# Performance work log

Measured on AMD Instinct MI355X. Metric: run time of the kernel, lower is better.

Reference implementation:

```python
import jax, jax.numpy as jnp
import numpy as np

N, E, IN_DIM, OUT_DIM, SEM_DIM = 50000, 800000, 128, 128, 128
EPS = 1e-8


def setup_inputs() -> dict:
    key = jax.random.key(0)
    k = jax.random.split(key, 8)
    x = jax.random.normal(k[0], (N, IN_DIM), dtype=jnp.float32)
    edge_index = jax.random.randint(k[1], (2, E), 0, N, dtype=jnp.int64)
    semantic_vec = jax.random.normal(k[2], (N, SEM_DIM), dtype=jnp.float32)
    s = 1.0 / np.sqrt(IN_DIM)
    W_src = jax.random.uniform(k[3], (OUT_DIM, IN_DIM), jnp.float32, -s, s)
    b_src = jax.random.uniform(k[4], (OUT_DIM,), jnp.float32, -s, s)
    W_dst = jax.random.uniform(k[5], (OUT_DIM, IN_DIM), jnp.float32, -s, s)
    b_dst = jax.random.uniform(k[6], (OUT_DIM,), jnp.float32, -s, s)
    return {"x": x, "edge_index": edge_index, "semantic_vec": semantic_vec,
            "W_src": W_src, "b_src": b_src, "W_dst": W_dst, "b_dst": b_dst}


def _scatter_softmax(sim, dst, num_segments):
    # numerically stable segment-wise softmax over edges grouped by dst
    seg_max = jax.ops.segment_max(sim, dst, num_segments=num_segments)
    seg_max = jnp.where(jnp.isneginf(seg_max), 0.0, seg_max)
    e = jnp.exp(sim - seg_max[dst])
    seg_sum = jax.ops.segment_sum(e, dst, num_segments=num_segments)
    return e / (seg_sum[dst] + 1e-16)


def reference(x, edge_index, semantic_vec, W_src, b_src, W_dst, b_dst):
    src, dst = edge_index[0], edge_index[1]
    x_j = x[src] @ W_src.T + b_src           # [E, out_dim]
    # cosine similarity with torch eps semantics
    a = semantic_vec[src]
    b = semantic_vec[dst]
    na = jnp.maximum(jnp.linalg.norm(a, axis=-1), EPS)
    nb = jnp.maximum(jnp.linalg.norm(b, axis=-1), EPS)
    sim = jnp.sum(a * b, axis=-1) / (na * nb)  # [E]
    attn = _scatter_softmax(sim, dst, x.shape[0])
    msg = attn[:, None] * x_j                 # [E, out_dim]
    out = jax.ops.segment_sum(msg, dst, num_segments=x.shape[0])
    return out
```

## Files before the change

### kernel.cpp

```cpp
#include <hip/hip_runtime.h>
#include <hip/hip_fp16.h>

#define Nn 50000
#define Ee 800000
#define D  128
#define SLOT 64

typedef _Float16 f16x8 __attribute__((ext_vector_type(8)));
typedef _Float16 h2    __attribute__((ext_vector_type(2)));
typedef float    f32x4 __attribute__((ext_vector_type(4)));


__global__ __launch_bounds__(256) void k_zero(int* __restrict__ cnt) {
  int i = blockIdx.x * 256 + threadIdx.x;
  *(int4*)(cnt + i * 4) = (int4){0, 0, 0, 0};
}

__global__ __launch_bounds__(256) void k_scat(const int* __restrict__ ei,
                                              int* __restrict__ cnt,
                                              unsigned short* __restrict__ slot16) {
  int t = blockIdx.x * 256 + threadIdx.x;
  int e0 = t * 4;
  if (e0 >= Ee) return;
  int4 s4 = *(const int4*)(ei + e0);
  int4 d4 = *(const int4*)(ei + Ee + e0);
  int ss[4] = {s4.x, s4.y, s4.z, s4.w};
  int dd[4] = {d4.x, d4.y, d4.z, d4.w};
#pragma unroll
  for (int u = 0; u < 4; u++) {
    int e = e0 + u;
    if (e < Ee) {
      int pos = atomicAdd(cnt + dd[u], 1);
      if (pos < SLOT)
        slot16[(size_t)dd[u] * SLOT + pos] = (unsigned short)ss[u];
    }
  }
}

__global__ __launch_bounds__(256) void k_node(const float* __restrict__ x,
                                              const float* __restrict__ W,
                                              const float* __restrict__ b,
                                              const float* __restrict__ sem,
                                              __half* __restrict__ blob) {
  __shared__ __half sW16[128 * 136] __attribute__((aligned(16)));
  int bid = blockIdx.x, tid = threadIdx.x;
  int n0 = bid * 32;
  int wave = tid >> 6, lane = tid & 63;

  for (int r = 0; r < 16; r++) {
    int i = tid + 256 * r;
    int row = i >> 5, c4 = (i & 31) << 2;
    float4 w = *(const float4*)(W + (size_t)row * 128 + c4);
    __half2* dst = (__half2*)&sW16[row * 136 + c4];
    dst[0] = __floats2half2_rn(w.x, w.y);
    dst[1] = __floats2half2_rn(w.z, w.w);
  }

#pragma unroll
  for (int it = 0; it < 8; it++) {
    int n = n0 + it * 4 + wave;
    if (n < Nn) {
      const float2 v = *(const float2*)(sem + (size_t)n * D + 2 * lane);
      float p = v.x * v.x + v.y * v.y;
#pragma unroll
      for (int off = 32; off > 0; off >>= 1) p += __shfl_xor(p, off);
      float inv = 1.0f / fmaxf(sqrtf(p), 1e-8f);
      *(__half2*)(blob + (size_t)n * 256 + 2 * lane) = __floats2half2_rn(v.x * inv, v.y * inv);
    }
  }

  int rs = (wave >> 1) * 16;
  int ch = (wave & 1) * 64;
  int g = lane >> 4, n16 = lane & 15;

  int arow = n0 + rs + n16; if (arow >= Nn) arow = Nn - 1;
  const float* xr = x + (size_t)arow * 128 + g * 8;
  union { f16x8 v; __half2 h[4]; } af[4];
#pragma unroll
  for (int kt = 0; kt < 4; kt++) {
    float4 u0 = *(const float4*)(xr + kt * 32);
    float4 u1 = *(const float4*)(xr + kt * 32 + 4);
    af[kt].h[0] = __floats2half2_rn(u0.x, u0.y);
    af[kt].h[1] = __floats2half2_rn(u0.z, u0.w);
    af[kt].h[2] = __floats2half2_rn(u1.x, u1.y);
    af[kt].h[3] = __floats2half2_rn(u1.z, u1.w);
  }

  __syncthreads();

  f32x4 acc[4];
#pragma unroll
  for (int jt = 0; jt < 4; jt++) {
    float bias = b[ch + jt * 16 + n16];
    acc[jt] = (f32x4){bias, bias, bias, bias};
  }
#pragma unroll
  for (int kt = 0; kt < 4; kt++) {
#pragma unroll
    for (int jt = 0; jt < 4; jt++) {
      f16x8 bf = *(const f16x8*)(&sW16[(ch + jt * 16 + n16) * 136 + kt * 32 + g * 8]);
      acc[jt] = __builtin_amdgcn_mfma_f32_16x16x32_f16(af[kt].v, bf, acc[jt], 0, 0, 0);
    }
  }
#pragma unroll
  for (int jt = 0; jt < 4; jt++) {
#pragma unroll
    for (int rr = 0; rr < 4; rr++) {
      int row = n0 + rs + g * 4 + rr;
      if (row < Nn)
        blob[(size_t)row * 256 + 128 + ch + jt * 16 + n16] = __float2half(acc[jt][rr]);
    }
  }
}

__global__ __launch_bounds__(256) void k_fused(const __half* __restrict__ blob,
                                               const unsigned short* __restrict__ slot16,
                                               const int* __restrict__ cnt,
                                               float* __restrict__ out) {
  int d = (blockIdx.x * 256 + threadIdx.x) >> 6;
  int lane = threadIdx.x & 63;
  int g = lane >> 4, l16 = lane & 15;
  int c = cnt[d]; if (c > SLOT) c = SLOT;

  int sv = (lane < c) ? (int)slot16[(size_t)d * SLOT + lane] : 0;

  f16x8 dh = *(const f16x8*)(blob + (size_t)d * 256 + l16 * 8);

  float o[8] = {0, 0, 0, 0, 0, 0, 0, 0};
  float Sp = 0.0f;

  for (int i = 0; i < c; i += 4) {
    int e = i + g;
    int ce = e < c ? e : c - 1;
    int sa = __shfl(sv, ce);
    const __half* nbp = blob + (size_t)sa * 256;
    f16x8 rs = *(const f16x8*)(nbp + l16 * 8);
    f16x8 ry = *(const f16x8*)(nbp + 128 + l16 * 8);
    float p = __builtin_amdgcn_fdot2((h2){rs[0], rs[1]}, (h2){dh[0], dh[1]}, 0.0f, false);
    p = __builtin_amdgcn_fdot2((h2){rs[2], rs[3]}, (h2){dh[2], dh[3]}, p, false);
    p = __builtin_amdgcn_fdot2((h2){rs[4], rs[5]}, (h2){dh[4], dh[5]}, p, false);
    p = __builtin_amdgcn_fdot2((h2){rs[6], rs[7]}, (h2){dh[6], dh[7]}, p, false);
    p += __shfl_xor(p, 1); p += __shfl_xor(p, 2);
    p += __shfl_xor(p, 4); p += __shfl_xor(p, 8);
    float ew = __expf(p); if (e >= c) ew = 0.0f;
    Sp += ew;
#pragma unroll
    for (int k = 0; k < 8; k++) o[k] += ew * (float)ry[k];
  }

#pragma unroll
  for (int k = 0; k < 8; k++) {
    o[k] += __shfl_xor(o[k], 16);
    o[k] += __shfl_xor(o[k], 32);
  }
  Sp += __shfl_xor(Sp, 16);
  Sp += __shfl_xor(Sp, 32);

  if (g == 0) {
    float inv = 1.0f / (Sp + 1e-16f);
    float4 r0; r0.x = o[0] * inv; r0.y = o[1] * inv; r0.z = o[2] * inv; r0.w = o[3] * inv;
    float4 r1; r1.x = o[4] * inv; r1.y = o[5] * inv; r1.z = o[6] * inv; r1.w = o[7] * inv;
    float* op = out + (size_t)d * D + l16 * 8;
    *(float4*)op = r0;
    *(float4*)(op + 4) = r1;
  }
}

extern "C" void kernel_launch(void* const* d_in, const int* in_sizes, int n_in,
                              void* d_out, int out_size, void* d_ws, size_t ws_size,
                              hipStream_t stream) {
  const float* x     = (const float*)d_in[0];
  const int*   ei    = (const int*)d_in[1];
  const float* sem   = (const float*)d_in[2];
  const float* W_src = (const float*)d_in[3];
  const float* b_src = (const float*)d_in[4];
  float* out = (float*)d_out;

  char* ws = (char*)d_ws;
  const size_t O_BLOB = 0;
  const size_t O_CNT  = 25600000;
  const size_t O_SS   = 25804800;
  const size_t NEED   = 32204800;
  if (ws_size < NEED) return;

  __half* blob = (__half*)(ws + O_BLOB);
  int* cnt = (int*)(ws + O_CNT);
  unsigned short* slot16 = (unsigned short*)(ws + O_SS);

  k_zero<<<49, 256, 0, stream>>>(cnt);
  k_scat<<<782, 256, 0, stream>>>(ei, cnt, slot16);
  k_node<<<1563, 256, 0, stream>>>(x, W_src, b_src, sem, blob);
  k_fused<<<(Nn + 3) / 4, 256, 0, stream>>>(blob, slot16, cnt, out);
}
```

Before: 217.5 us.

## Merge edge scatter and node transform into one kernel, prefetch neighbor rows

Combines the edge-bucketing scatter and the node projection/normalization kernels into one launch, with even blocks doing edge atomics and odd blocks doing the MFMA node work, so the two independent phases overlap and one launch is saved. The shared-memory weight row stride drops from 136 to 132 halves. The aggregation loop now software-prefetches the next group of neighbor rows before computing the current one, to hide gather latency. The cost is more registers in the gather loop and a possible change in LDS bank-conflict behaviour from the new padding.

```diff
diff --git a/kernel.cpp b/kernel.cpp
--- a/kernel.cpp
+++ b/kernel.cpp
@@ -16,42 +16,41 @@
   *(int4*)(cnt + i * 4) = (int4){0, 0, 0, 0};
 }
 
-__global__ __launch_bounds__(256) void k_scat(const int* __restrict__ ei,
-                                              int* __restrict__ cnt,
-                                              unsigned short* __restrict__ slot16) {
-  int t = blockIdx.x * 256 + threadIdx.x;
-  int e0 = t * 4;
-  if (e0 >= Ee) return;
-  int4 s4 = *(const int4*)(ei + e0);
-  int4 d4 = *(const int4*)(ei + Ee + e0);
-  int ss[4] = {s4.x, s4.y, s4.z, s4.w};
-  int dd[4] = {d4.x, d4.y, d4.z, d4.w};
-#pragma unroll
-  for (int u = 0; u < 4; u++) {
-    int e = e0 + u;
-    if (e < Ee) {
-      int pos = atomicAdd(cnt + dd[u], 1);
-      if (pos < SLOT)
-        slot16[(size_t)dd[u] * SLOT + pos] = (unsigned short)ss[u];
-    }
-  }
-}
-
-__global__ __launch_bounds__(256) void k_node(const float* __restrict__ x,
-                                              const float* __restrict__ W,
-                                              const float* __restrict__ b,
-                                              const float* __restrict__ sem,
-                                              __half* __restrict__ blob) {
-  __shared__ __half sW16[128 * 136] __attribute__((aligned(16)));
+__global__ __launch_bounds__(256) void k_phaseA(const float* __restrict__ x,
+                                                const float* __restrict__ W,
+                                                const float* __restrict__ b,
+                                                const int* __restrict__ ei,
+                                                const float* __restrict__ sem,
+                                                __half* __restrict__ blob,
+                                                int* __restrict__ cnt,
+                                                unsigned short* __restrict__ slot16) {
+  __shared__ __half sW16[128 * 132] __attribute__((aligned(16)));
   int bid = blockIdx.x, tid = threadIdx.x;
-  int n0 = bid * 32;
+
+  if ((bid & 1) == 0) {
+    int base = (bid >> 1) * 512 + tid;
+#pragma unroll
+    for (int u = 0; u < 2; u++) {
+      int e = base + u * 256;
+      if (e < Ee) {
+        int s = ei[e], d = ei[Ee + e];
+        int pos = atomicAdd(cnt + d, 1);
+        if (pos < SLOT)
+          slot16[(size_t)d * SLOT + pos] = (unsigned short)s;
+      }
+    }
+    return;
+  }
+
+  int nb = bid >> 1;
+  int n0 = nb * 32;
   int wave = tid >> 6, lane = tid & 63;
 
   for (int r = 0; r < 16; r++) {
     int i = tid + 256 * r;
     int row = i >> 5, c4 = (i & 31) << 2;
     float4 w = *(const float4*)(W + (size_t)row * 128 + c4);
-    __half2* dst = (__half2*)&sW16[row * 136 + c4];
+    __half2* dst = (__half2*)&sW16[row * 132 + c4];
     dst[0] = __floats2half2_rn(w.x, w.y);
     dst[1] = __floats2half2_rn(w.z, w.w);
   }
@@ -98,7 +97,7 @@
   for (int kt = 0; kt < 4; kt++) {
 #pragma unroll
     for (int jt = 0; jt < 4; jt++) {
-      f16x8 bf = *(const f16x8*)(&sW16[(ch + jt * 16 + n16) * 136 + kt * 32 + g * 8]);
+      f16x8 bf = *(const f16x8*)(&sW16[(ch + jt * 16 + n16) * 132 + kt * 32 + g * 8]);
       acc[jt] = __builtin_amdgcn_mfma_f32_16x16x32_f16(af[kt].v, bf, acc[jt], 0, 0, 0);
     }
   }
@@ -129,20 +128,32 @@
   float o[8] = {0, 0, 0, 0, 0, 0, 0, 0};
   float Sp = 0.0f;
 
-  for (int i = 0; i < c; i += 4) {
-    int e = i + g;
-    int ce = e < c ? e : c - 1;
+  f16x8 rs0, ry0;
+  if (c > 0) {
+    int ce = (g < c) ? g : c - 1;
     int sa = __shfl(sv, ce);
     const __half* nbp = blob + (size_t)sa * 256;
-    f16x8 rs = *(const f16x8*)(nbp + l16 * 8);
-    f16x8 ry = *(const f16x8*)(nbp + 128 + l16 * 8);
+    rs0 = *(const f16x8*)(nbp + l16 * 8);
+    ry0 = *(const f16x8*)(nbp + 128 + l16 * 8);
+  }
+
+  for (int i = 0; i < c; i += 4) {
+    f16x8 rs = rs0, ry = ry0;
+    if (i + 4 < c) {
+      int e2 = i + 4 + g;
+      int ce2 = (e2 < c) ? e2 : c - 1;
+      int sa2 = __shfl(sv, ce2);
+      const __half* nb2 = blob + (size_t)sa2 * 256;
+      rs0 = *(const f16x8*)(nb2 + l16 * 8);
+      ry0 = *(const f16x8*)(nb2 + 128 + l16 * 8);
+    }
     float p = __builtin_amdgcn_fdot2((h2){rs[0], rs[1]}, (h2){dh[0], dh[1]}, 0.0f, false);
     p = __builtin_amdgcn_fdot2((h2){rs[2], rs[3]}, (h2){dh[2], dh[3]}, p, false);
     p = __builtin_amdgcn_fdot2((h2){rs[4], rs[5]}, (h2){dh[4], dh[5]}, p, false);
     p = __builtin_amdgcn_fdot2((h2){rs[6], rs[7]}, (h2){dh[6], dh[7]}, p, false);
     p += __shfl_xor(p, 1); p += __shfl_xor(p, 2);
     p += __shfl_xor(p, 4); p += __shfl_xor(p, 8);
-    float ew = __expf(p); if (e >= c) ew = 0.0f;
+    float ew = __expf(p); if (i + g >= c) ew = 0.0f;
     Sp += ew;
 #pragma unroll
     for (int k = 0; k < 8; k++) o[k] += ew * (float)ry[k];
@@ -187,8 +198,7 @@
   int* cnt = (int*)(ws + O_CNT);
   unsigned short* slot16 = (unsigned short*)(ws + O_SS);
 
-  k_zero<<<49, 256, 0, stream>>>(cnt);
-  k_scat<<<782, 256, 0, stream>>>(ei, cnt, slot16);
-  k_node<<<1563, 256, 0, stream>>>(x, W_src, b_src, sem, blob);
-  k_fused<<<(Nn + 3) / 4, 256, 0, stream>>>(blob, slot16, cnt, out);
-}
+  k_zero<<<50, 256, 0, stream>>>(cnt);
+  k_phaseA<<<3126, 256, 0, stream>>>(x, W_src, b_src, ei, sem, blob, cnt, slot16);
+  k_fused<<<12500, 256, 0, stream>>>(blob, slot16, cnt, out);
+}
```

Result: faster. 203.9 us (-6.3%).
